# Kernel tuning notes

Hardware: AMD Instinct MI355X
Metric: run time of the kernel (lower is better)

Reference implementation:

```python
import jax, jax.numpy as jnp
import numpy as np

B, N_NODE, N_TOK = 8, 512, 8
N_PATHS, PATH_LEN = 256, 64
VOCAB, H = 50000, 256


def gru_dir(x, w_ih, w_hh, b_ih, b_hh):
    # x: [batch, T, H_in] -> [batch, T, H]; PyTorch GRU gate math
    xw = jnp.einsum('bti,gi->btg', x, w_ih) + b_ih  # precompute input-side gates
    h0 = jnp.zeros((x.shape[0], w_hh.shape[1]), x.dtype)
    def step(h, xt):
        gh = h @ w_hh.T + b_hh
        xr, xz, xn = jnp.split(xt, 3, -1)
        hr, hz, hn = jnp.split(gh, 3, -1)
        r = jax.nn.sigmoid(xr + hr)
        z = jax.nn.sigmoid(xz + hz)
        n = jnp.tanh(xn + r * hn)
        h_new = (1.0 - z) * n + z * h
        return h_new, h_new
    _, ys = jax.lax.scan(step, h0, jnp.swapaxes(xw, 0, 1))
    return jnp.swapaxes(ys, 0, 1)


def gru_bidir(x, wf_ih, wf_hh, bf_ih, bf_hh, wb_ih, wb_hh, bb_ih, bb_hh):
    f = gru_dir(x, wf_ih, wf_hh, bf_ih, bf_hh)
    b = jnp.flip(gru_dir(jnp.flip(x, 1), wb_ih, wb_hh, bb_ih, bb_hh), 1)
    return jnp.concatenate([f, b], -1)


def setup_inputs():
    key = jax.random.key(0)
    ks = jax.random.split(key, 18)
    g = lambda k, s: jax.random.normal(k, s, jnp.float32) * 0.06
    return {
        'nodes': jax.random.randint(ks[0], (B, N_NODE, N_TOK), 0, VOCAB),
        'paths': jax.random.randint(ks[1], (B, N_PATHS, PATH_LEN), 0, N_NODE + 1),
        'emb': g(ks[2], (VOCAB, H)),
        'wf_ih': g(ks[3], (3 * H, H)), 'wf_hh': g(ks[4], (3 * H, H)),
        'bf_ih': g(ks[5], (3 * H,)), 'bf_hh': g(ks[6], (3 * H,)),
        'wb_ih': g(ks[7], (3 * H, H)), 'wb_hh': g(ks[8], (3 * H, H)),
        'bb_ih': g(ks[9], (3 * H,)), 'bb_hh': g(ks[10], (3 * H,)),
        'w_transit': g(ks[11], (2 * H, H)), 'b_transit': g(ks[12], (2 * H,)),
        'w_rank': g(ks[13], (2 * H, 2 * H + 1)), 'b_rank': g(ks[14], (2 * H,)),
        'w_h': g(ks[15], (H, 2 * H)), 'b_h': g(ks[16], (H,)),
    }


def reference(nodes, paths, emb, wf_ih, wf_hh, bf_ih, bf_hh, wb_ih, wb_hh, bb_ih, bb_hh, w_transit, b_transit, w_rank, b_rank, w_h, b_h):
    gru = (wf_ih, wf_hh, bf_ih, bf_hh, wb_ih, wb_hh, bb_ih, bb_hh)
    x = jnp.max(emb[nodes], axis=2)                 # [B, N_NODE, H] token max-pool
    base_v = gru_bidir(x, *gru)                     # [B, N_NODE, 2H]
    x_pad = jnp.concatenate([x, jnp.zeros((B, 1, H), x.dtype)], axis=1)
    gathered = jax.vmap(lambda xp, p: xp[p])(x_pad, paths)        # [B, P, L, H]
    nx = gru_bidir(gathered.reshape(B * N_PATHS, PATH_LEN, H), *gru)
    nx = nx.reshape(B, N_PATHS, PATH_LEN, 2 * H)
    # extra rank feature: 1/(path_index+1), broadcast over path positions
    rank = (1.0 / (jnp.arange(N_PATHS, dtype=x.dtype) + 1.0))[None, :, None, None]
    rank = jnp.broadcast_to(rank, (B, N_PATHS, PATH_LEN, 1))
    nx = jnp.concatenate([nx, rank], -1) @ w_rank.T + b_rank      # rank_proj
    p_flat = paths.reshape(B, -1)
    v_flat = nx.reshape(B, N_PATHS * PATH_LEN, 2 * H)
    def pool(pf, vf, xb):
        # scatter-max per node id; id N_NODE is the padding row and is dropped
        vmax = jnp.full((N_NODE + 1, 2 * H), -jnp.inf, vf.dtype).at[pf].max(vf)
        has = jnp.zeros((N_NODE + 1,), bool).at[pf].set(True)
        fallback = xb @ w_transit.T + b_transit
        return jnp.where(has[:N_NODE, None], vmax[:N_NODE], fallback)
    v = jax.vmap(pool)(p_flat, v_flat, x)           # [B, N_NODE, 2H]
    all_v = base_v + v
    last_state = jnp.max(all_v, axis=1) @ w_h.T + b_h             # h_proj branch (GRU -> not tuple)
    return all_v, last_state
```

## Files before the change

kernel.cpp:

```cpp
#include <hip/hip_runtime.h>


#define HH 256
#define NNODE 512
#define PLEN 64

typedef __attribute__((ext_vector_type(8))) short short8;
typedef __attribute__((ext_vector_type(4))) float f32x4;
typedef unsigned short ushort_t;
typedef __attribute__((address_space(1))) const void* gas_t;
typedef __attribute__((address_space(3))) void* las_t;

__device__ __forceinline__ f32x4 mfma16(short8 a, short8 b, f32x4 c) {
    return __builtin_amdgcn_mfma_f32_16x16x32_bf16(a, b, c, 0, 0, 0);
}
__device__ __forceinline__ ushort_t f2bf(float f) {
    unsigned u = __float_as_uint(f);
    u += 0x7fffu + ((u >> 16) & 1u);
    return (ushort_t)(u >> 16);
}
__device__ __forceinline__ float bf2f(ushort_t s) {
    return __uint_as_float(((unsigned)s) << 16);
}
__device__ __forceinline__ float sigm(float x) {
    return __builtin_amdgcn_rcpf(1.f + __expf(-x));
}
__device__ __forceinline__ float tanh_(float x) {
    return 1.f - 2.f * __builtin_amdgcn_rcpf(__expf(2.f * x) + 1.f);
}
__device__ __forceinline__ unsigned fkey(float f) {
    unsigned u = __float_as_uint(f);
    return (u & 0x80000000u) ? ~u : (u | 0x80000000u);
}
__device__ __forceinline__ float fdec(unsigned k) {
    unsigned u = (k & 0x80000000u) ? (k ^ 0x80000000u) : ~k;
    return __uint_as_float(u);
}

__device__ __forceinline__ int xw3_remap(int c) {
    const int dir = c >= 768;
    const int cd = c - dir * 768;
    const int g = cd >> 8, cc = cd & 255;
    const int w2 = cc >> 5, within = cc & 31;
    return dir * 768 + w2 * 96 + (within >> 1) * 6 + g * 2 + (within & 1);
}

__global__ void k_embed(const int* __restrict__ nodes, const float* __restrict__ emb,
                        float* __restrict__ x, ushort_t* __restrict__ xbf)
{
    const int bn = blockIdx.x, h = threadIdx.x;
    const int* nd = nodes + bn * 8;
    float m = -3.4e38f;
#pragma unroll
    for (int k = 0; k < 8; ++k)
        m = fmaxf(m, emb[(size_t)nd[k] * HH + h]);
    x[(size_t)bn * HH + h] = m;
    xbf[(size_t)bn * HH + h] = f2bf(m);
}

__global__ void k_pack(const float* __restrict__ wf_ih, const float* __restrict__ wf_hh,
                       const float* __restrict__ bf_ih, const float* __restrict__ bf_hh,
                       const float* __restrict__ wb_ih, const float* __restrict__ wb_hh,
                       const float* __restrict__ bb_ih, const float* __restrict__ bb_hh,
                       const float* __restrict__ w_rank,
                       ushort_t* __restrict__ whhp, ushort_t* __restrict__ wih_bt,
                       ushort_t* __restrict__ wr_bt, float* __restrict__ rank_l,
                       float* __restrict__ bias2, ushort_t* __restrict__ xw3)
{
    int i = blockIdx.x * 256 + threadIdx.x;
    if (i < 393216) {
        const int e = i & 7, l = (i >> 3) & 63;
        const int c = i >> 9;
        const int q = c % 48;
        const int w2 = (c / 48) & 7;
        const int dir = c / 384;
        int kt, g;
        if (q < 12)      { kt = q / 6;            g = (q % 6) >> 1; }
        else if (q < 24) { kt = 2 + (q - 12) / 6; g = ((q - 12) % 6) >> 1; }
        else if (q < 28) { kt = 4;                g = (q - 24) >> 1; }
        else if (q < 30) { kt = 4;                g = 2; }
        else             { kt = 5 + (q - 30) / 6; g = ((q - 30) % 6) >> 1; }
        const int n = q & 1;
        const float* whh = dir ? wb_hh : wf_hh;
        whhp[i] = f2bf(whh[(g * 256 + w2 * 32 + 2 * (l & 15) + n) * 256 +
                           kt * 32 + (l >> 4) * 8 + e]);
        return;
    }
    i -= 393216;
    if (i < 393216) {
        const int n = i >> 8, k = i & 255;
        const float* wih = (n < 768) ? wf_ih : wb_ih;
        wih_bt[i] = f2bf(wih[(n % 768) * 256 + k]);
        return;
    }
    i -= 393216;
    if (i < 262144) { wr_bt[i] = f2bf(w_rank[(i >> 9) * 513 + (i & 511)]); return; }
    i -= 262144;
    if (i < 512) { rank_l[i] = w_rank[i * 513 + 512]; return; }
    i -= 512;
    if (i < 1536) {
        const int c = i;
        const int dir = c >= 768;
        const int cd = c - dir * 768;
        const int g = cd >> 8;
        const float bi = dir ? bb_ih[cd] : bf_ih[cd];
        const float bh = (g < 2) ? (dir ? bb_hh[cd] : bf_hh[cd]) : 0.f;
        bias2[c] = bi + bh;
        xw3[(size_t)4096 * 1536 + xw3_remap(c)] = f2bf(bi + bh);
    }
}

template<int KD>
__device__ __forceinline__ void gemm_loop(const ushort_t* __restrict__ A,
                                          const ushort_t* __restrict__ Bt,
                                          ushort_t* al, ushort_t* bl,
                                          int bm, int bn, f32x4 acc[4][4])
{
    const int tid = threadIdx.x, w = tid >> 6, l = tid & 63;
    const int lm = l & 15, lh = l >> 4;
    const int wm = w >> 1, wn = w & 1;
    const int lr = l >> 3, lc = (l & 7) * 8;
    for (int k0 = 0; k0 < KD; k0 += 64) {
#pragma unroll
        for (int i = 0; i < 4; ++i) {
            const int c = w * 4 + i;
            const ushort_t* ga = A + (size_t)(bm + c * 8 + lr) * KD + k0 + lc;
            const ushort_t* gb = Bt + (size_t)(bn + c * 8 + lr) * KD + k0 + lc;
            __builtin_amdgcn_global_load_lds((gas_t)ga, (las_t)(al + c * 512), 16, 0, 0);
            __builtin_amdgcn_global_load_lds((gas_t)gb, (las_t)(bl + c * 512), 16, 0, 0);
        }
        __syncthreads();
#pragma unroll
        for (int kt = 0; kt < 2; ++kt) {
            short8 af[4], bfr[4];
            const int ko = kt * 32 + lh * 8;
#pragma unroll
            for (int m = 0; m < 4; ++m)
                af[m] = *(const short8*)(al + (wm * 64 + m * 16 + lm) * 64 + ko);
#pragma unroll
            for (int n = 0; n < 4; ++n)
                bfr[n] = *(const short8*)(bl + (wn * 64 + n * 16 + lm) * 64 + ko);
#pragma unroll
            for (int m = 0; m < 4; ++m)
#pragma unroll
                for (int n = 0; n < 4; ++n)
                    acc[m][n] = mfma16(af[m], bfr[n], acc[m][n]);
        }
        __syncthreads();
    }
}

__global__ void __launch_bounds__(256, 2)
k_gemm_xw(const ushort_t* __restrict__ xbf, const ushort_t* __restrict__ wih_bt,
          const float* __restrict__ bias2, ushort_t* __restrict__ xw3)
{
    __shared__ __align__(16) ushort_t al[128 * 64], bl[128 * 64];
    f32x4 acc[4][4] = {};
    const int bm = blockIdx.y * 128, bn = blockIdx.x * 128;
    gemm_loop<256>(xbf, wih_bt, al, bl, bm, bn, acc);
    const int tid = threadIdx.x, w = tid >> 6, l = tid & 63;
    const int lm = l & 15, lh = l >> 4, wm = w >> 1, wn = w & 1;
#pragma unroll
    for (int m = 0; m < 4; ++m)
#pragma unroll
        for (int rr = 0; rr < 4; ++rr) {
            const int row = bm + wm * 64 + m * 16 + lh * 4 + rr;
#pragma unroll
            for (int n = 0; n < 4; ++n) {
                const int col = bn + wn * 64 + n * 16 + lm;
                xw3[(size_t)row * 1536 + xw3_remap(col)] = f2bf(acc[m][n][rr] + bias2[col]);
            }
        }
}

template<bool IS_BASE>
__device__ __forceinline__ void scan_run(int dir, int sg, int tid,
    const ushort_t* __restrict__ xw3, const ushort_t* __restrict__ whhp,
    const float* __restrict__ bhh, ushort_t* __restrict__ wl,
    ushort_t (*hl)[4096], const int* idr,
    ushort_t* __restrict__ nx, float* __restrict__ base_v)
{
    const int w = tid >> 6, l = tid & 63;
    const int lm = l & 15, lh = l >> 4;
    const int nsteps = IS_BASE ? NNODE : PLEN;
    const ushort_t* wp = whhp + ((size_t)(dir * 8 + w) * 48) * 512 + l * 8;

    short8 Breg[12];
#pragma unroll
    for (int q = 0; q < 12; ++q) {
        short8 v = *(const short8*)(wp + q * 512);
        asm volatile("" : "+v"(v));
        Breg[q] = v;
    }
#pragma unroll
    for (int q = 12; q < 28; ++q)
        __builtin_amdgcn_global_load_lds((gas_t)(wp + q * 512),
            (las_t)(wl + ((q - 12) * 8 + w) * 512), 16, 0, 0);

    const float bn0 = bhh[512 + w * 32 + lm * 2];
    const float bn1 = bhh[512 + w * 32 + lm * 2 + 1];

    __syncthreads();
    for (int i = tid; i < 4096; i += 512) hl[0][i] = 0;
    __syncthreads();

    int cur = 0;
    for (int step = 0; step < nsteps; ++step) {
        const int t = dir ? (nsteps - 1 - step) : step;
        uint3 gv[4];
#pragma unroll
        for (int ri = 0; ri < 4; ++ri) {
            const int sq = lh * 4 + ri;
            const int row = IS_BASE ? ((sq < 8) ? ((sq << 9) + t) : 4096)
                                    : idr[(sq << 6) + t];
            gv[ri] = *(const uint3*)((const char*)xw3 +
                (size_t)row * 3072 + dir * 1536 + w * 192 + lm * 12);
        }
        short8 st[8];
#pragma unroll
        for (int j = 0; j < 8; ++j) st[j] = *(const short8*)(wp + (28 + j) * 512);

        f32x4 acc[3][2] = {};
        const char* hb = (const char*)hl[cur];
        short8 af;
#pragma unroll
        for (int kt = 0; kt < 2; ++kt) {
            af = *(const short8*)(hb + lm * 512 + ((kt * 64 + lh * 16) ^ ((lm & 7) << 4)));
#pragma unroll
            for (int j = 0; j < 6; ++j)
                acc[j >> 1][j & 1] = mfma16(af, Breg[kt * 6 + j], acc[j >> 1][j & 1]);
        }
#pragma unroll
        for (int kt = 2; kt < 4; ++kt) {
            af = *(const short8*)(hb + lm * 512 + ((kt * 64 + lh * 16) ^ ((lm & 7) << 4)));
            const int fb = (kt - 2) * 6;
#pragma unroll
            for (int j = 0; j < 6; ++j) {
                const short8 b = *(const short8*)(wl + ((fb + j) * 8 + w) * 512 + l * 8);
                acc[j >> 1][j & 1] = mfma16(af, b, acc[j >> 1][j & 1]);
            }
        }
        af = *(const short8*)(hb + lm * 512 + ((4 * 64 + lh * 16) ^ ((lm & 7) << 4)));
#pragma unroll
        for (int j = 0; j < 4; ++j) {
            const short8 b = *(const short8*)(wl + ((12 + j) * 8 + w) * 512 + l * 8);
            acc[j >> 1][j & 1] = mfma16(af, b, acc[j >> 1][j & 1]);
        }
        acc[2][0] = mfma16(af, st[0], acc[2][0]);
        acc[2][1] = mfma16(af, st[1], acc[2][1]);
        af = *(const short8*)(hb + lm * 512 + ((5 * 64 + lh * 16) ^ ((lm & 7) << 4)));
#pragma unroll
        for (int j = 0; j < 6; ++j)
            acc[j >> 1][j & 1] = mfma16(af, st[2 + j], acc[j >> 1][j & 1]);
#pragma unroll
        for (int j = 0; j < 6; ++j) st[2 + j] = *(const short8*)(wp + (36 + j) * 512);
        af = *(const short8*)(hb + lm * 512 + ((6 * 64 + lh * 16) ^ ((lm & 7) << 4)));
#pragma unroll
        for (int j = 0; j < 6; ++j)
            acc[j >> 1][j & 1] = mfma16(af, st[2 + j], acc[j >> 1][j & 1]);
#pragma unroll
        for (int j = 0; j < 6; ++j) st[2 + j] = *(const short8*)(wp + (42 + j) * 512);
        af = *(const short8*)(hb + lm * 512 + ((7 * 64 + lh * 16) ^ ((lm & 7) << 4)));
#pragma unroll
        for (int j = 0; j < 6; ++j)
            acc[j >> 1][j & 1] = mfma16(af, st[2 + j], acc[j >> 1][j & 1]);

        ushort_t* hn_ = hl[cur ^ 1];
#pragma unroll
        for (int ri = 0; ri < 4; ++ri) {
            const int sq = lh * 4 + ri;
            const unsigned hv = *(const unsigned*)(hb + sq * 512 +
                ((w * 64 + lm * 4) ^ ((sq & 7) << 4)));
            unsigned hpack = 0;
            float hs0 = 0.f, hs1 = 0.f;
#pragma unroll
            for (int n = 0; n < 2; ++n) {
                const float xr = bf2f((ushort_t)(n ? (gv[ri].x >> 16) : (gv[ri].x & 0xffffu)));
                const float xz = bf2f((ushort_t)(n ? (gv[ri].y >> 16) : (gv[ri].y & 0xffffu)));
                const float xn = bf2f((ushort_t)(n ? (gv[ri].z >> 16) : (gv[ri].z & 0xffffu)));
                const float hov = bf2f((ushort_t)(n ? (hv >> 16) : (hv & 0xffffu)));
                const float rr = sigm(acc[0][n][ri] + xr);
                const float zz = sigm(acc[1][n][ri] + xz);
                const float nn = tanh_(xn + rr * (acc[2][n][ri] + (n ? bn1 : bn0)));
                const float h = (1.f - zz) * nn + zz * hov;
                if (n) hs1 = h; else hs0 = h;
                hpack |= ((unsigned)f2bf(h)) << (n * 16);
            }
            *(unsigned*)((char*)hn_ + sq * 512 + ((w * 64 + lm * 4) ^ ((sq & 7) << 4))) = hpack;
            if (IS_BASE) {
                if (sq < 8)
                    *(float2*)(base_v + ((size_t)(sq * NNODE + t)) * 512 +
                               dir * 256 + w * 32 + lm * 2) = make_float2(hs0, hs1);
            } else {
                *(unsigned*)((char*)nx + (((size_t)((sg * 16 + sq) * PLEN + t)) * 512 +
                    dir * 256 + w * 32 + lm * 2) * 2) = hpack;
            }
        }
        __syncthreads();
        cur ^= 1;
    }
}

__global__ void __launch_bounds__(512)
k_scan(const int* __restrict__ paths, const ushort_t* __restrict__ xw3,
       const ushort_t* __restrict__ whhp,
       const float* __restrict__ bf_hh, const float* __restrict__ bb_hh,
       const ushort_t* __restrict__ wr_bt, const float* __restrict__ b_rank,
       const float* __restrict__ rank_l,
       ushort_t* __restrict__ nx, float* __restrict__ base_v,
       unsigned* __restrict__ keys)
{
    __shared__ __align__(16) ushort_t wl[65536];
    __shared__ __align__(16) ushort_t hl[2][4096];
    __shared__ int idr[1024];
    const int tid = threadIdx.x;
    const int w = tid >> 6, l = tid & 63;
    const int lm = l & 15, lh = l >> 4;

    if (blockIdx.x < 2) {
        scan_run<true>((int)blockIdx.x, 0, tid, xw3, whhp,
                       blockIdx.x ? bb_hh : bf_hh, wl, hl, nullptr, nx, base_v);
        return;
    }
    const int sg = (int)blockIdx.x - 2;
    for (int i = tid; i < 1024; i += 512) {
        const int s = sg * 16 + (i >> 6), t = i & 63;
        const int id = paths[(s << 6) + t];
        idr[i] = (id < NNODE) ? (((s >> 8) << 9) + id) : 4096;
    }
    scan_run<false>(0, sg, tid, xw3, whhp, bf_hh, wl, hl, idr, nx, base_v);
    scan_run<false>(1, sg, tid, xw3, whhp, bb_hh, wl, hl, idr, nx, base_v);

    __threadfence_block();
    __syncthreads();
    ushort_t* al = wl;
    ushort_t* bl = wl + 8192;
    const int wm = w >> 2, wn = w & 3;
#pragma unroll 1
    for (int job = 0; job < 32; ++job) {
        const int mt = job >> 2, ntile = job & 3;
        const size_t ar0 = (size_t)sg * 1024 + mt * 128;
        const int n0 = ntile * 128;
        f32x4 racc[4][2] = {};
        for (int k0 = 0; k0 < 512; k0 += 64) {
#pragma unroll
            for (int i = 0; i < 2; ++i) {
                const int c = w * 128 + i * 64 + l;
                const int row = c >> 3, j = c & 7;
                const int jp = j ^ (row & 7);
                __builtin_amdgcn_global_load_lds(
                    (gas_t)(nx + (ar0 + row) * 512 + k0 + jp * 8),
                    (las_t)(al + c * 8), 16, 0, 0);
                __builtin_amdgcn_global_load_lds(
                    (gas_t)(wr_bt + (size_t)(n0 + row) * 512 + k0 + jp * 8),
                    (las_t)(bl + c * 8), 16, 0, 0);
            }
            __syncthreads();
#pragma unroll
            for (int kt = 0; kt < 2; ++kt) {
                short8 av[4], bv[2];
#pragma unroll
                for (int m = 0; m < 4; ++m) {
                    const int r = wm * 64 + m * 16 + lm;
                    av[m] = *(const short8*)((const char*)al + r * 128 +
                            ((kt * 64 + lh * 16) ^ ((r & 7) << 4)));
                }
#pragma unroll
                for (int n = 0; n < 2; ++n) {
                    const int r = wn * 32 + n * 16 + lm;
                    bv[n] = *(const short8*)((const char*)bl + r * 128 +
                            ((kt * 64 + lh * 16) ^ ((r & 7) << 4)));
                }
#pragma unroll
                for (int m = 0; m < 4; ++m)
#pragma unroll
                    for (int n = 0; n < 2; ++n)
                        racc[m][n] = mfma16(av[m], bv[n], racc[m][n]);
            }
            __syncthreads();
        }
#pragma unroll
        for (int m = 0; m < 4; ++m)
#pragma unroll
            for (int rr = 0; rr < 4; ++rr) {
                const size_t grow = ar0 + wm * 64 + m * 16 + lh * 4 + rr;
                const int id = paths[grow];
                const float rv = __builtin_amdgcn_rcpf((float)(((grow >> 6) & 255) + 1));
                unsigned* kp = keys + (((grow >> 14) * 513 + id) << 9);
#pragma unroll
                for (int n = 0; n < 2; ++n) {
                    const int col = n0 + wn * 32 + n * 16 + lm;
                    const float v = racc[m][n][rr] + b_rank[col] + rank_l[col] * rv;
                    if (id < NNODE) {
                        const unsigned key = fkey(v);
                        if (key > kp[col]) atomicMax(kp + col, key);
                    }
                }
            }
    }
}

__global__ void k_merge(const unsigned* __restrict__ keys, const float* __restrict__ base_v,
                        const float* __restrict__ x, const float* __restrict__ w_transit,
                        const float* __restrict__ b_transit, float* __restrict__ out0)
{
    const int blk = blockIdx.x;
    const int b = blk >> 9, n = blk & 511;
    const int tid = threadIdx.x;
#pragma unroll
    for (int h = 0; h < 2; ++h) {
        const int o = tid + h * 256;
        const unsigned k = keys[((size_t)(b * 513 + n)) * 512 + o];
        float v;
        if (k) {
            v = fdec(k);
        } else {
            float a = b_transit[o];
            const float* wt = w_transit + o * HH;
            const float* xr = x + ((size_t)(b * NNODE + n)) * HH;
            for (int i = 0; i < HH; ++i) a += xr[i] * wt[i];
            v = a;
        }
        const size_t oi = ((size_t)(b * NNODE + n)) * 512 + o;
        out0[oi] = base_v[oi] + v;
    }
}

__global__ void k_last(const float* __restrict__ out0, const float* __restrict__ w_h,
                       const float* __restrict__ b_h, float* __restrict__ out1)
{
    __shared__ float m[512];
    const int b = blockIdx.x, tid = threadIdx.x;
#pragma unroll
    for (int h = 0; h < 2; ++h) {
        const int o = tid + h * 256;
        float mm = -3.4e38f;
        for (int n = 0; n < NNODE; ++n)
            mm = fmaxf(mm, out0[((size_t)(b * NNODE + n)) * 512 + o]);
        m[o] = mm;
    }
    __syncthreads();
    float a = b_h[tid];
    const float* wr = w_h + tid * 512;
    for (int j = 0; j < 512; ++j) a += m[j] * wr[j];
    out1[b * HH + tid] = a;
}

extern "C" void kernel_launch(void* const* d_in, const int* in_sizes, int n_in,
                              void* d_out, int out_size, void* d_ws, size_t ws_size,
                              hipStream_t stream)
{
    (void)in_sizes; (void)n_in; (void)out_size; (void)ws_size;
    const int* nodes = (const int*)d_in[0];
    const int* paths = (const int*)d_in[1];
    const float* emb = (const float*)d_in[2];
    const float* wf_ih = (const float*)d_in[3];
    const float* wf_hh = (const float*)d_in[4];
    const float* bf_ih = (const float*)d_in[5];
    const float* bf_hh = (const float*)d_in[6];
    const float* wb_ih = (const float*)d_in[7];
    const float* wb_hh = (const float*)d_in[8];
    const float* bb_ih = (const float*)d_in[9];
    const float* bb_hh = (const float*)d_in[10];
    const float* w_transit = (const float*)d_in[11];
    const float* b_transit = (const float*)d_in[12];
    const float* w_rank = (const float*)d_in[13];
    const float* b_rank = (const float*)d_in[14];
    const float* w_h = (const float*)d_in[15];
    const float* b_h = (const float*)d_in[16];

    char* ws = (char*)d_ws;
    float* x = (float*)(ws);
    ushort_t* xbf = (ushort_t*)(ws + 4194304);
    ushort_t* xw3 = (ushort_t*)(ws + 6291456);
    ushort_t* whhp = (ushort_t*)(ws + 18877440);
    ushort_t* wih_bt = (ushort_t*)(ws + 19663872);
    ushort_t* wr_bt = (ushort_t*)(ws + 20450304);
    float* rank_l = (float*)(ws + 20974592);
    float* bias2 = (float*)(ws + 20976640);
    unsigned* keys = (unsigned*)(ws + 20982784);
    float* base_v = (float*)(ws + 29387776);
    ushort_t* nx = (ushort_t*)(ws + 37776384);

    float* out0 = (float*)d_out;
    float* out1 = out0 + 2097152;

    hipMemsetAsync(keys, 0, 8404992, stream);
    k_embed<<<4096, 256, 0, stream>>>(nodes, emb, x, xbf);
    k_pack<<<4104, 256, 0, stream>>>(wf_ih, wf_hh, bf_ih, bf_hh, wb_ih, wb_hh,
                                     bb_ih, bb_hh, w_rank,
                                     whhp, wih_bt, wr_bt, rank_l, bias2, xw3);
    k_gemm_xw<<<dim3(12, 32), 256, 0, stream>>>(xbf, wih_bt, bias2, xw3);
    k_scan<<<130, 512, 0, stream>>>(paths, xw3, whhp, bf_hh, bb_hh, wr_bt,
                                    b_rank, rank_l, nx, base_v, keys);
    k_merge<<<4096, 256, 0, stream>>>(keys, base_v, x, w_transit, b_transit, out0);
    k_last<<<8, 256, 0, stream>>>(out0, w_h, b_h, out1);
}
```

Measured before the change: 1.887 ms.

## Split base-sequence GRU scan across two blocks with cross-block flag sync

The 512-step base GRU scan per direction now runs on two cooperating workgroups, each computing half of the hidden columns. The halves exchange new hidden state every step through a global buffer and release/acquire flags. The goal is to shorten the serial critical path, since the long base scan likely dominates k_scan while the path scans are short. In exchange it adds a global round trip and a spin-wait per step, depends on all four blocks being co-resident to avoid deadlock, and reuses the wih_bt workspace region for pbuf and flags after the GEMM has finished with it.

```diff
diff --git a/kernel.cpp b/kernel.cpp
--- a/kernel.cpp
+++ b/kernel.cpp
@@ -173,16 +173,131 @@
         }
 }
 
-template<bool IS_BASE>
-__device__ __forceinline__ void scan_run(int dir, int sg, int tid,
+__device__ __forceinline__ void base_run(int dir, int half, int tid,
+    const ushort_t* __restrict__ xw3, const float* __restrict__ whh,
+    const float* __restrict__ bhh, ushort_t* __restrict__ wl,
+    ushort_t (*hl)[4096], float* __restrict__ pbuf, unsigned* __restrict__ flags,
+    float* __restrict__ base_v)
+{
+    const int w = tid >> 6, l = tid & 63;
+    const int lm = l & 15, lh = l >> 4;
+    const int hcol = half * 128 + w * 16 + lm;
+    const int kk = lh * 8;
+
+    short8 Breg[12];
+#pragma unroll
+    for (int kt = 0; kt < 4; ++kt)
+#pragma unroll
+        for (int g = 0; g < 3; ++g) {
+            const float* src = whh + (size_t)(g * 256 + hcol) * 256 + kt * 32 + kk;
+            short8 v;
+#pragma unroll
+            for (int e = 0; e < 8; ++e) v[e] = (short)f2bf(src[e]);
+            asm volatile("" : "+v"(v));
+            Breg[kt * 3 + g] = v;
+        }
+#pragma unroll
+    for (int kt = 4; kt < 8; ++kt)
+#pragma unroll
+        for (int g = 0; g < 3; ++g) {
+            const float* src = whh + (size_t)(g * 256 + hcol) * 256 + kt * 32 + kk;
+            short8 v;
+#pragma unroll
+            for (int e = 0; e < 8; ++e) v[e] = (short)f2bf(src[e]);
+            *(short8*)(wl + ((size_t)(((kt - 4) * 3 + g) * 8 + w)) * 512 + l * 8) = v;
+        }
+    const float bn_ = bhh[512 + hcol];
+    const int goff = dir * 768 + (hcol >> 5) * 96 + ((hcol & 31) >> 1) * 6 + (hcol & 1);
+
+    unsigned* flag_own = flags + (dir * 2 + half) * 32;
+    unsigned* flag_par = flags + (dir * 2 + (1 - half)) * 32;
+    float* pb_own = pbuf + (dir * 2 + half) * 2048;
+    const float* pb_par = pbuf + (dir * 2 + (1 - half)) * 2048;
+    const int ph = 1 - half;
+
+    __syncthreads();
+    for (int i = tid; i < 4096; i += 512) hl[0][i] = 0;
+    __syncthreads();
+
+    int cur = 0;
+    for (int step = 0; step < NNODE; ++step) {
+        const int t = dir ? (NNODE - 1 - step) : step;
+        if (step) {
+            while (__hip_atomic_load(flag_par, __ATOMIC_ACQUIRE,
+                                     __HIP_MEMORY_SCOPE_AGENT) < (unsigned)step) {}
+            const float* src = pb_par + ((step - 1) & 1) * 1024;
+#pragma unroll
+            for (int i2 = 0; i2 < 2; ++i2) {
+                const int i = tid * 2 + i2;
+                const int row = i >> 7, c = i & 127;
+                const float v = __hip_atomic_load(src + i, __ATOMIC_RELAXED,
+                                                  __HIP_MEMORY_SCOPE_AGENT);
+                const int col = ph * 128 + c;
+                *(ushort_t*)((char*)hl[cur] + row * 512 +
+                             ((col * 2) ^ ((row & 7) << 4))) = f2bf(v);
+            }
+        }
+        __syncthreads();
+        ushort_t gr[4], gz[4], gn[4];
+#pragma unroll
+        for (int ri = 0; ri < 4; ++ri) {
+            const int sq = lh * 4 + ri;
+            const int row = (sq < 8) ? ((sq << 9) + t) : 4096;
+            const ushort_t* gp = xw3 + (size_t)row * 1536 + goff;
+            gr[ri] = gp[0]; gz[ri] = gp[2]; gn[ri] = gp[4];
+        }
+        f32x4 acc[3] = {};
+        const char* hb = (const char*)hl[cur];
+#pragma unroll
+        for (int kt = 0; kt < 4; ++kt) {
+            const short8 a = *(const short8*)(hb + lm * 512 +
+                ((kt * 64 + lh * 16) ^ ((lm & 7) << 4)));
+            acc[0] = mfma16(a, Breg[kt * 3 + 0], acc[0]);
+            acc[1] = mfma16(a, Breg[kt * 3 + 1], acc[1]);
+            acc[2] = mfma16(a, Breg[kt * 3 + 2], acc[2]);
+        }
+#pragma unroll
+        for (int kt = 4; kt < 8; ++kt) {
+            const short8 a = *(const short8*)(hb + lm * 512 +
+                ((kt * 64 + lh * 16) ^ ((lm & 7) << 4)));
+            const int fb = (kt - 4) * 3;
+            acc[0] = mfma16(a, *(const short8*)(wl + ((size_t)((fb + 0) * 8 + w)) * 512 + l * 8), acc[0]);
+            acc[1] = mfma16(a, *(const short8*)(wl + ((size_t)((fb + 1) * 8 + w)) * 512 + l * 8), acc[1]);
+            acc[2] = mfma16(a, *(const short8*)(wl + ((size_t)((fb + 2) * 8 + w)) * 512 + l * 8), acc[2]);
+        }
+        ushort_t* hn_ = hl[cur ^ 1];
+        float* pw = pb_own + (step & 1) * 1024;
+#pragma unroll
+        for (int ri = 0; ri < 4; ++ri) {
+            const int sq = lh * 4 + ri;
+            const int hoff = sq * 512 + ((hcol * 2) ^ ((sq & 7) << 4));
+            const float hov = bf2f(*(const ushort_t*)(hb + hoff));
+            const float rr = sigm(acc[0][ri] + bf2f(gr[ri]));
+            const float zz = sigm(acc[1][ri] + bf2f(gz[ri]));
+            const float nn = tanh_(bf2f(gn[ri]) + rr * (acc[2][ri] + bn_));
+            const float h = (1.f - zz) * nn + zz * hov;
+            *(ushort_t*)((char*)hn_ + hoff) = f2bf(h);
+            if (sq < 8) {
+                __hip_atomic_store(pw + sq * 128 + (hcol & 127), h,
+                                   __ATOMIC_RELAXED, __HIP_MEMORY_SCOPE_AGENT);
+                base_v[((size_t)(sq * NNODE + t)) * 512 + dir * 256 + hcol] = h;
+            }
+        }
+        __syncthreads();
+        if (tid == 0)
+            __hip_atomic_store(flag_own, (unsigned)(step + 1),
+                               __ATOMIC_RELEASE, __HIP_MEMORY_SCOPE_AGENT);
+        cur ^= 1;
+    }
+}
+
+__device__ __forceinline__ void path_run(int dir, int sg, int tid,
     const ushort_t* __restrict__ xw3, const ushort_t* __restrict__ whhp,
     const float* __restrict__ bhh, ushort_t* __restrict__ wl,
-    ushort_t (*hl)[4096], const int* idr,
-    ushort_t* __restrict__ nx, float* __restrict__ base_v)
+    ushort_t (*hl)[4096], const int* idr, ushort_t* __restrict__ nx)
 {
     const int w = tid >> 6, l = tid & 63;
     const int lm = l & 15, lh = l >> 4;
-    const int nsteps = IS_BASE ? NNODE : PLEN;
     const ushort_t* wp = whhp + ((size_t)(dir * 8 + w) * 48) * 512 + l * 8;
 
     short8 Breg[12];
@@ -205,14 +320,13 @@
     __syncthreads();
 
     int cur = 0;
-    for (int step = 0; step < nsteps; ++step) {
-        const int t = dir ? (nsteps - 1 - step) : step;
+    for (int step = 0; step < PLEN; ++step) {
+        const int t = dir ? (PLEN - 1 - step) : step;
         uint3 gv[4];
 #pragma unroll
         for (int ri = 0; ri < 4; ++ri) {
             const int sq = lh * 4 + ri;
-            const int row = IS_BASE ? ((sq < 8) ? ((sq << 9) + t) : 4096)
-                                    : idr[(sq << 6) + t];
+            const int row = idr[(sq << 6) + t];
             gv[ri] = *(const uint3*)((const char*)xw3 +
                 (size_t)row * 3072 + dir * 1536 + w * 192 + lm * 12);
         }
@@ -272,7 +386,6 @@
             const unsigned hv = *(const unsigned*)(hb + sq * 512 +
                 ((w * 64 + lm * 4) ^ ((sq & 7) << 4)));
             unsigned hpack = 0;
-            float hs0 = 0.f, hs1 = 0.f;
 #pragma unroll
             for (int n = 0; n < 2; ++n) {
                 const float xr = bf2f((ushort_t)(n ? (gv[ri].x >> 16) : (gv[ri].x & 0xffffu)));
@@ -283,18 +396,11 @@
                 const float zz = sigm(acc[1][n][ri] + xz);
                 const float nn = tanh_(xn + rr * (acc[2][n][ri] + (n ? bn1 : bn0)));
                 const float h = (1.f - zz) * nn + zz * hov;
-                if (n) hs1 = h; else hs0 = h;
                 hpack |= ((unsigned)f2bf(h)) << (n * 16);
             }
             *(unsigned*)((char*)hn_ + sq * 512 + ((w * 64 + lm * 4) ^ ((sq & 7) << 4))) = hpack;
-            if (IS_BASE) {
-                if (sq < 8)
-                    *(float2*)(base_v + ((size_t)(sq * NNODE + t)) * 512 +
-                               dir * 256 + w * 32 + lm * 2) = make_float2(hs0, hs1);
-            } else {
-                *(unsigned*)((char*)nx + (((size_t)((sg * 16 + sq) * PLEN + t)) * 512 +
-                    dir * 256 + w * 32 + lm * 2) * 2) = hpack;
-            }
+            *(unsigned*)((char*)nx + (((size_t)((sg * 16 + sq) * PLEN + t)) * 512 +
+                dir * 256 + w * 32 + lm * 2) * 2) = hpack;
         }
         __syncthreads();
         cur ^= 1;
@@ -304,11 +410,13 @@
 __global__ void __launch_bounds__(512)
 k_scan(const int* __restrict__ paths, const ushort_t* __restrict__ xw3,
        const ushort_t* __restrict__ whhp,
+       const float* __restrict__ wf_hh, const float* __restrict__ wb_hh,
        const float* __restrict__ bf_hh, const float* __restrict__ bb_hh,
        const ushort_t* __restrict__ wr_bt, const float* __restrict__ b_rank,
        const float* __restrict__ rank_l,
        ushort_t* __restrict__ nx, float* __restrict__ base_v,
-       unsigned* __restrict__ keys)
+       unsigned* __restrict__ keys, float* __restrict__ pbuf,
+       unsigned* __restrict__ flags)
 {
     __shared__ __align__(16) ushort_t wl[65536];
     __shared__ __align__(16) ushort_t hl[2][4096];
@@ -317,19 +425,20 @@
     const int w = tid >> 6, l = tid & 63;
     const int lm = l & 15, lh = l >> 4;
 
-    if (blockIdx.x < 2) {
-        scan_run<true>((int)blockIdx.x, 0, tid, xw3, whhp,
-                       blockIdx.x ? bb_hh : bf_hh, wl, hl, nullptr, nx, base_v);
+    if (blockIdx.x < 4) {
+        const int dir = blockIdx.x >> 1, half = blockIdx.x & 1;
+        base_run(dir, half, tid, xw3, dir ? wb_hh : wf_hh, dir ? bb_hh : bf_hh,
+                 wl, hl, pbuf, flags, base_v);
         return;
     }
-    const int sg = (int)blockIdx.x - 2;
+    const int sg = (int)blockIdx.x - 4;
     for (int i = tid; i < 1024; i += 512) {
         const int s = sg * 16 + (i >> 6), t = i & 63;
         const int id = paths[(s << 6) + t];
         idr[i] = (id < NNODE) ? (((s >> 8) << 9) + id) : 4096;
     }
-    scan_run<false>(0, sg, tid, xw3, whhp, bf_hh, wl, hl, idr, nx, base_v);
-    scan_run<false>(1, sg, tid, xw3, whhp, bb_hh, wl, hl, idr, nx, base_v);
+    path_run(0, sg, tid, xw3, whhp, bf_hh, wl, hl, idr, nx);
+    path_run(1, sg, tid, xw3, whhp, bb_hh, wl, hl, idr, nx);
 
     __threadfence_block();
     __syncthreads();
@@ -475,6 +584,8 @@
     ushort_t* xw3 = (ushort_t*)(ws + 6291456);
     ushort_t* whhp = (ushort_t*)(ws + 18877440);
     ushort_t* wih_bt = (ushort_t*)(ws + 19663872);
+    float* pbuf = (float*)(ws + 19663872);
+    unsigned* flags = (unsigned*)(ws + 19663872 + 32768);
     ushort_t* wr_bt = (ushort_t*)(ws + 20450304);
     float* rank_l = (float*)(ws + 20974592);
     float* bias2 = (float*)(ws + 20976640);
@@ -491,8 +602,10 @@
                                      bb_ih, bb_hh, w_rank,
                                      whhp, wih_bt, wr_bt, rank_l, bias2, xw3);
     k_gemm_xw<<<dim3(12, 32), 256, 0, stream>>>(xbf, wih_bt, bias2, xw3);
-    k_scan<<<130, 512, 0, stream>>>(paths, xw3, whhp, bf_hh, bb_hh, wr_bt,
-                                    b_rank, rank_l, nx, base_v, keys);
+    hipMemsetAsync(pbuf, 0, 33280, stream);
+    k_scan<<<132, 512, 0, stream>>>(paths, xw3, whhp, wf_hh, wb_hh, bf_hh, bb_hh,
+                                    wr_bt, b_rank, rank_l, nx, base_v, keys,
+                                    pbuf, flags);
     k_merge<<<4096, 256, 0, stream>>>(keys, base_v, x, w_transit, b_transit, out0);
     k_last<<<8, 256, 0, stream>>>(out0, w_h, b_h, out1);
 }
```

Result: slower. 2.599 ms (+37.7%).
